# Kernel optimization log

Measured on AMD Instinct MI355X. Metric: run time of the kernel, lower is better.

## Reference

```python
import jax, jax.numpy as jnp
import numpy as np
from jax import lax

B = 1
D, H, W = 16, 16, 32
L = D * H * W
C = 96          # hidden_dim
DIN = 96        # d_inner = expansion_factor(1) * hidden_dim
N = 16          # d_state
R = 6           # dt_rank = ceil(C / 16)
K = 8           # scan directions: 4 axis orders x {fwd, bwd}
PERMS = [(0, 1, 2), (1, 2, 0), (2, 0, 1), (2, 1, 0)]


def _ln(x, w, b, eps):
    m = x.mean(-1, keepdims=True)
    v = ((x - m) ** 2).mean(-1, keepdims=True)
    return (x - m) * lax.rsqrt(v + eps) * w + b


def _conv3d(x, w, b, groups=1):
    y = lax.conv_general_dilated(x, w, (1, 1, 1), 'SAME', feature_group_count=groups,
                                 dimension_numbers=('NCDHW', 'OIDHW', 'NCDHW'))
    return y + b[None, :, None, None, None]


def _ss3d(x5, in_proj_w, conv_w, conv_b, x_proj_w, dt_w, dt_b, A_logs, Ds,
          out_norm_w, out_norm_b, out_proj_w):
    b, d, h, w, _ = x5.shape
    l = d * h * w
    spatial = (d, h, w)
    xz = jnp.einsum('bdhwc,ec->bdhwe', x5, in_proj_w)          # (b,d,h,w,2*DIN)
    x, z = jnp.split(xz, 2, axis=-1)
    x = jnp.transpose(x, (0, 4, 1, 2, 3))                       # (b,DIN,d,h,w)
    x = jax.nn.silu(_conv3d(x, conv_w, conv_b, groups=DIN))     # depthwise conv
    # build K/2 axis-order scans, then add reversed copies -> K directions
    xs = jnp.stack([jnp.transpose(x, (0, 1, 2 + p[0], 2 + p[1], 2 + p[2])).reshape(b, DIN, l)
                    for p in PERMS], axis=1)                    # (b,4,DIN,l)
    xs = jnp.concatenate([xs, jnp.flip(xs, -1)], axis=1)        # (b,K,DIN,l)
    x_dbl = jnp.einsum('bkdl,ked->bkel', xs, x_proj_w)          # e = R+2N
    dts, Bs, Cs = x_dbl[:, :, :R], x_dbl[:, :, R:R + N], x_dbl[:, :, R + N:]
    dts = jax.nn.softplus(jnp.einsum('bkrl,kdr->bkdl', dts, dt_w) + dt_b[None, :, :, None])
    A = -jnp.exp(A_logs)                                        # (K,DIN,N)
    # time-major for the selective scan
    dts_t = jnp.moveaxis(dts, -1, 0)                            # (l,b,K,DIN)
    xs_t = jnp.moveaxis(xs, -1, 0)
    Bs_t = jnp.moveaxis(Bs, -1, 0)                              # (l,b,K,N)
    Cs_t = jnp.moveaxis(Cs, -1, 0)

    def step(hc, inps):
        dt, u, Bt, Ct = inps
        hc = jnp.exp(dt[..., None] * A) * hc + (dt * u)[..., None] * Bt[:, :, None, :]
        y = jnp.einsum('bkdn,bkn->bkd', hc, Ct)
        return hc, y

    h0 = jnp.zeros((b, K, DIN, N), x.dtype)
    _, ys = lax.scan(step, h0, (dts_t, xs_t, Bs_t, Cs_t))       # ys: (l,b,K,DIN)
    ys = jnp.moveaxis(ys, 0, -1) + Ds[None, :, :, None] * xs    # (b,K,DIN,l)
    y_f, y_b = ys[:, :4], jnp.flip(ys[:, 4:], -1)
    acc = jnp.zeros((b, DIN, l), x.dtype)
    for i, p in enumerate(PERMS):
        inv = np.argsort(p)
        pshape = tuple(spatial[ax] for ax in p)
        for yk in (y_f[:, i], y_b[:, i]):
            yk = yk.reshape(b, DIN, *pshape)
            yk = jnp.transpose(yk, (0, 1, 2 + int(inv[0]), 2 + int(inv[1]), 2 + int(inv[2])))
            acc = acc + yk.reshape(b, DIN, l)
    y = _ln(jnp.transpose(acc, (0, 2, 1)), out_norm_w, out_norm_b, 1e-5)
    y = y.reshape(b, d, h, w, DIN) * jax.nn.silu(z)
    return jnp.einsum('bdhwe,ce->bdhwc', y, out_proj_w)


def _cab(x, cab_w1, cab_b1, cab_w2, cab_b2, ca_w1, ca_b1, ca_w2, ca_b2):
    # x: (b,C,d,h,w); conv -> GELU -> conv -> channel attention
    t = jax.nn.gelu(_conv3d(x, cab_w1, cab_b1), approximate=False)
    t = _conv3d(t, cab_w2, cab_b2)
    m = t.mean(axis=(2, 3, 4))                                  # global avg pool (b,C)
    v = jax.nn.relu(m @ ca_w1.T + ca_b1)
    v = jax.nn.sigmoid(v @ ca_w2.T + ca_b2)
    return t * v[:, :, None, None, None]


def _forward(inp, ln1_w, ln1_b, skip1, skip2, ln2_w, ln2_b, in_proj_w, conv_w, conv_b,
             x_proj_w, dt_w, dt_b, A_logs, Ds, out_norm_w, out_norm_b, out_proj_w,
             cab_w1, cab_b1, cab_w2, cab_b2, ca_w1, ca_b1, ca_w2, ca_b2, x_size):
    b, l, c = inp.shape
    d, h, w = x_size
    x5 = inp.reshape(b, d, h, w, c)
    xn = _ln(x5, ln1_w, ln1_b, 1e-6)
    attn = _ss3d(xn, in_proj_w, conv_w, conv_b, x_proj_w, dt_w, dt_b, A_logs, Ds,
                 out_norm_w, out_norm_b, out_proj_w)
    x = x5 * skip1 + attn                                       # drop_path = identity (rate 0)
    y2 = jnp.transpose(_ln(x, ln2_w, ln2_b, 1e-5), (0, 4, 1, 2, 3))
    cab = _cab(y2, cab_w1, cab_b1, cab_w2, cab_b2, ca_w1, ca_b1, ca_w2, ca_b2)
    x = x * skip2 + jnp.transpose(cab, (0, 2, 3, 4, 1))
    return x.reshape(b, l, c)


def setup_inputs() -> dict:
    key = jax.random.key(0)
    ks = jax.random.split(key, 12)
    g = lambda i, shp, s=0.02: jax.random.normal(ks[i], shp, jnp.float32) * s
    return {
        'inp': jax.random.normal(ks[0], (B, L, C), jnp.float32),
        'x_size': (D, H, W),
        'ln1_w': jnp.ones((C,), jnp.float32), 'ln1_b': jnp.zeros((C,), jnp.float32),
        'skip1': jnp.ones((C,), jnp.float32), 'skip2': jnp.ones((C,), jnp.float32),
        'ln2_w': jnp.ones((C,), jnp.float32), 'ln2_b': jnp.zeros((C,), jnp.float32),
        'in_proj_w': g(1, (2 * DIN, C)),
        'conv_w': g(2, (DIN, 1, 3, 3, 3), 0.1), 'conv_b': jnp.zeros((DIN,), jnp.float32),
        'x_proj_w': g(3, (K, R + 2 * N, DIN)),
        'dt_w': g(4, (K, DIN, R), 0.1), 'dt_b': g(5, (K, DIN), 0.1),
        'A_logs': jnp.log(jnp.tile(jnp.arange(1, N + 1, dtype=jnp.float32), (K, DIN, 1))),
        'Ds': jnp.ones((K, DIN), jnp.float32),
        'out_norm_w': jnp.ones((DIN,), jnp.float32), 'out_norm_b': jnp.zeros((DIN,), jnp.float32),
        'out_proj_w': g(6, (C, DIN)),
        'cab_w1': g(7, (C // 3, C, 3, 3, 3), 0.05), 'cab_b1': jnp.zeros((C // 3,), jnp.float32),
        'cab_w2': g(8, (C, C // 3, 3, 3, 3), 0.05), 'cab_b2': jnp.zeros((C,), jnp.float32),
        'ca_w1': g(9, (C // 2, C)), 'ca_b1': jnp.zeros((C // 2,), jnp.float32),
        'ca_w2': g(10, (C, C // 2)), 'ca_b2': jnp.zeros((C,), jnp.float32),
    }


def reference(inp, ln1_w, ln1_b, skip1, skip2, ln2_w, ln2_b, in_proj_w, conv_w, conv_b,
              x_proj_w, dt_w, dt_b, A_logs, Ds, out_norm_w, out_norm_b, out_proj_w,
              cab_w1, cab_b1, cab_w2, cab_b2, ca_w1, ca_b1, ca_w2, ca_b2, x_size):
    return _forward(inp, ln1_w, ln1_b, skip1, skip2, ln2_w, ln2_b, in_proj_w, conv_w, conv_b,
                    x_proj_w, dt_w, dt_b, A_logs, Ds, out_norm_w, out_norm_b, out_proj_w,
                    cab_w1, cab_b1, cab_w2, cab_b2, ca_w1, ca_b1, ca_w2, ca_b2, x_size)
```

## Files before the change

### kernel.cpp

```cpp
#include <hip/hip_runtime.h>
#include <math.h>

#define LL 8192
#define CC 96
#define DINc 96
#define NN 16
#define RR 6
#define KK 8
#define Dd 16
#define Hh 16
#define Ww 32
#define NCH 32
#define CHL 256

__constant__ int Pc_[4][3] = {{0,1,2},{1,2,0},{2,0,1},{2,1,0}};

__device__ __forceinline__ float silu_(float x){ return x / (1.f + __expf(-x)); }

__global__ void k_ln1(const float* __restrict__ inp, const float* __restrict__ w,
                      const float* __restrict__ b, float* __restrict__ xn_cm) {
    int l = blockIdx.x * blockDim.x + threadIdx.x;
    if (l >= LL) return;
    const float* p = inp + l * CC;
    float m = 0.f;
    for (int c = 0; c < CC; ++c) m += p[c];
    m *= (1.f / CC);
    float v = 0.f;
    for (int c = 0; c < CC; ++c) { float d = p[c] - m; v += d * d; }
    v *= (1.f / CC);
    float r = rsqrtf(v + 1e-6f);
    for (int c = 0; c < CC; ++c) xn_cm[c * LL + l] = (p[c] - m) * r * w[c] + b[c];
}

__global__ void k_wtrans(const float* __restrict__ inpj, const float* __restrict__ xpw,
                         const float* __restrict__ w1, const float* __restrict__ w2,
                         const float* __restrict__ opw,
                         float* __restrict__ ipT, float* __restrict__ xpT,
                         float* __restrict__ wT1, float* __restrict__ wT2,
                         float* __restrict__ opT) {
    int idx = blockIdx.x * blockDim.x + threadIdx.x;
    if (idx < 82944) {
        int oc = idx & 31; int tap = (idx >> 5) % 27; int ic = idx / (32 * 27);
        wT1[idx] = w1[(oc * 96 + ic) * 27 + tap];
    }
    if (idx < 82944) {
        int oc = idx % 96; int tap = (idx / 96) % 27; int ic = idx / (96 * 27);
        wT2[idx] = w2[(oc * 32 + ic) * 27 + tap];
    }
    if (idx < 18432) {
        int e = idx % 192; int c = idx / 192;
        ipT[idx] = inpj[e * 96 + c];
    }
    if (idx < 29184) {
        int e = idx % 38; int c = (idx / 38) % 96; int k = idx / (38 * 96);
        xpT[idx] = xpw[(k * 38 + e) * 96 + c];
    }
    if (idx < 9216) {
        int c = idx % 96; int e = idx / 96;
        opT[idx] = opw[c * 96 + e];
    }
}

__global__ void k_inproj(const float* __restrict__ xn_cm, const float* __restrict__ ipT,
                         float* __restrict__ xcm, float* __restrict__ z_rm) {
    int bx = blockIdx.x;
    int eb = bx >> 5;
    int l  = ((bx & 31) << 8) + threadIdx.x;
    int e0 = eb << 3;
    float a[8];
    #pragma unroll
    for (int j = 0; j < 8; ++j) a[j] = 0.f;
    const float* wp = ipT + e0;
    for (int c = 0; c < CC; ++c) {
        float x = xn_cm[c * LL + l];
        const float4* wv = (const float4*)(wp + c * 192);
        float4 wa = wv[0], wb = wv[1];
        a[0] += x * wa.x; a[1] += x * wa.y; a[2] += x * wa.z; a[3] += x * wa.w;
        a[4] += x * wb.x; a[5] += x * wb.y; a[6] += x * wb.z; a[7] += x * wb.w;
    }
    if (e0 < DINc) {
        float* dst = xcm + (long)e0 * LL;
        #pragma unroll
        for (int j = 0; j < 8; ++j) dst[(long)j * LL + l] = a[j];
    } else {
        float* dst = z_rm + (long)l * DINc + (e0 - DINc);
        #pragma unroll
        for (int j = 0; j < 8; ++j) dst[j] = a[j];
    }
}

__global__ void k_dwconv(const float* __restrict__ xcm, const float* __restrict__ cw,
                         const float* __restrict__ cb, float* __restrict__ xs0) {
    int bx = blockIdx.x;
    int c  = bx >> 3;
    int l4 = ((bx & 7) << 8) + threadIdx.x;
    int w0 = (l4 & 7) << 2;
    int h  = (l4 >> 3) & 15;
    int d  = l4 >> 7;
    int l  = (d * Hh + h) * Ww + w0;
    float wk[27];
    #pragma unroll
    for (int t = 0; t < 27; ++t) wk[t] = cw[c * 27 + t];
    float rmask[9]; int roff[9];
    #pragma unroll
    for (int kd = 0; kd < 3; ++kd) {
        int dd = d + kd - 1;
        bool vd = (unsigned)dd < Dd; int dc = vd ? dd : 0;
        #pragma unroll
        for (int kh = 0; kh < 3; ++kh) {
            int hh = h + kh - 1;
            bool vh = (unsigned)hh < Hh; int hcl = vh ? hh : 0;
            rmask[kd * 3 + kh] = (vd && vh) ? 1.f : 0.f;
            roff[kd * 3 + kh]  = (dc * Hh + hcl) * Ww + w0;
        }
    }
    float mleft  = (w0 > 0)  ? 1.f : 0.f;
    float mright = (w0 < 28) ? 1.f : 0.f;
    float a0 = cb[c], a1 = a0, a2 = a0, a3 = a0;
    const float* xp = xcm + (long)c * LL;
    #pragma unroll
    for (int r = 0; r < 9; ++r) {
        float rm = rmask[r];
        const float* xr = xp + roff[r];
        float4 xc = *(const float4*)xr;
        float v[6];
        v[0] = xr[-1] * (rm * mleft);
        v[1] = xc.x * rm; v[2] = xc.y * rm; v[3] = xc.z * rm; v[4] = xc.w * rm;
        v[5] = xr[4] * (rm * mright);
        #pragma unroll
        for (int t = 0; t < 3; ++t) {
            float wv = wk[r * 3 + t];
            a0 += v[t + 0] * wv;
            a1 += v[t + 1] * wv;
            a2 += v[t + 2] * wv;
            a3 += v[t + 3] * wv;
        }
    }
    *(float4*)(xs0 + (long)c * LL + l) = make_float4(silu_(a0), silu_(a1), silu_(a2), silu_(a3));
}

__global__ void k_permA(float* __restrict__ xs) {
    int idx = blockIdx.x * blockDim.x + threadIdx.x;
    if (idx >= 3 * DINc * LL) return;
    int l = idx & (LL - 1);
    int c = (idx >> 13) % DINc;
    int k = idx / (DINc * LL) + 1;
    int p0 = Pc_[k][0], p1 = Pc_[k][1], p2 = Pc_[k][2];
    const int sp[3] = {Dd, Hh, Ww};
    int pd1 = sp[p1], pd2 = sp[p2];
    int i2 = l % pd2;
    int t  = l / pd2;
    int i1 = t % pd1;
    int i0 = t / pd1;
    int coord[3];
    coord[p0] = i0; coord[p1] = i1; coord[p2] = i2;
    int o = (coord[0] * Hh + coord[1]) * Ww + coord[2];
    xs[(k * DINc + c) * LL + l] = xs[c * LL + o];
}

__global__ void k_permB(float* __restrict__ xs) {
    int idx = blockIdx.x * blockDim.x + threadIdx.x;
    if (idx >= 4 * DINc * (LL / 4)) return;
    int q = idx & (LL / 4 - 1);
    int c = (idx >> 11) % DINc;
    int k = idx / (DINc * (LL / 4));
    const float4* src = (const float4*)(xs + ((long)k * DINc + c) * LL);
    float4 s = src[LL / 4 - 1 - q];
    float4* dst = (float4*)(xs + ((long)(k + 4) * DINc + c) * LL);
    dst[q] = make_float4(s.w, s.z, s.y, s.x);
}

__global__ void k_xdbl(const float* __restrict__ xs, const float* __restrict__ xpT,
                       float* __restrict__ dtr, float* __restrict__ Bb, float* __restrict__ Cb) {
    int bx = blockIdx.x;
    int k = bx >> 5;
    int l = ((bx & 31) << 8) + threadIdx.x;
    float acc[38];
    #pragma unroll
    for (int e = 0; e < 38; ++e) acc[e] = 0.f;
    const float* xb = xs + (long)k * DINc * LL + l;
    const float* wb = xpT + k * DINc * 38;
    for (int c = 0; c < DINc; ++c) {
        float x = xb[(long)c * LL];
        const float* wr = wb + c * 38;
        #pragma unroll
        for (int e = 0; e < 38; ++e) acc[e] += x * wr[e];
    }
    float* dtp = dtr + ((long)k * LL + l) * 6;
    #pragma unroll
    for (int r = 0; r < RR; ++r) dtp[r] = acc[r];
    int lq = l >> 2, q = l & 3;
    float* Bp = Bb + (((long)k * 2048 + lq) * 16) * 4 + q;
    float* Cp = Cb + (((long)k * 2048 + lq) * 16) * 4 + q;
    #pragma unroll
    for (int n = 0; n < NN; ++n) { Bp[n * 4] = acc[RR + n]; Cp[n * 4] = acc[RR + NN + n]; }
}

__device__ __forceinline__ float softplus_(float x) {
    return (x > 20.f) ? x : __logf(1.f + __expf(x));
}

__global__ __launch_bounds__(512)
void k_scanf(float* __restrict__ xs_ys, const float* __restrict__ dtr,
             const float* __restrict__ Bb, const float* __restrict__ Cb,
             const float* __restrict__ A_logs, const float* __restrict__ dt_w,
             const float* __restrict__ dt_b, const float* __restrict__ Ds) {
    __shared__ __align__(16) float sdt[LL + (LL >> 7) * 4];
    __shared__ float sAp[16][33];
    __shared__ float sBc[16][33];
    __shared__ float shs[16][33];
    int bx = blockIdx.x;
    int grp = (bx & 7) * DINc + (bx >> 3);
    int k = grp / DINc;
    int tid = threadIdx.x;
    int n = tid & 15;
    int chunk = tid >> 4;
    {
        float w0 = dt_w[grp * RR + 0], w1 = dt_w[grp * RR + 1], w2 = dt_w[grp * RR + 2];
        float w3 = dt_w[grp * RR + 3], w4 = dt_w[grp * RR + 4], w5 = dt_w[grp * RR + 5];
        float dtb = dt_b[grp];
        const float* drb = dtr + (long)k * LL * 6;
        for (int i = tid; i < LL; i += 512) {
            const float2* dp = (const float2*)(drb + (long)i * 6);
            float2 d0 = dp[0], d1 = dp[1], d2 = dp[2];
            float dtl = dtb + d0.x * w0 + d0.y * w1 + d1.x * w2 + d1.y * w3 + d2.x * w4 + d2.y * w5;
            sdt[i + ((i >> 7) << 2)] = softplus_(dtl);
        }
    }
    __syncthreads();
    float A_n = -__expf(A_logs[grp * NN + n]);
    const float4* sdt4 = (const float4*)sdt;
    int dbase = chunk * 66;
    const float4* u4 = (const float4*)(xs_ys + (long)grp * LL + chunk * CHL);
    const float4* B4 = (const float4*)Bb + ((long)k * 2048 + chunk * (CHL / 4)) * 16 + n;
    const float4* C4 = (const float4*)Cb + ((long)k * 2048 + chunk * (CHL / 4)) * 16 + n;
    {
        float hc = 0.f, dsum = 0.f;
        #pragma unroll 4
        for (int q = 0; q < CHL / 4; ++q) {
            float4 dt = sdt4[dbase + q + (q >> 5)];
            float4 uu = u4[q];
            float4 Bv = B4[q * 16];
            dsum += (dt.x + dt.y) + (dt.z + dt.w);
            hc = __expf(dt.x * A_n) * hc + (dt.x * uu.x) * Bv.x;
            hc = __expf(dt.y * A_n) * hc + (dt.y * uu.y) * Bv.y;
            hc = __expf(dt.z * A_n) * hc + (dt.z * uu.z) * Bv.z;
            hc = __expf(dt.w * A_n) * hc + (dt.w * uu.w) * Bv.w;
        }
        sAp[n][chunk] = __expf(A_n * dsum);
        sBc[n][chunk] = hc;
    }
    __syncthreads();
    if (tid < 16) {
        float h = 0.f;
        for (int c = 0; c < NCH; ++c) {
            shs[tid][c] = h;
            h = sAp[tid][c] * h + sBc[tid][c];
        }
    }
    __syncthreads();
    float Dv = Ds[grp];
    float* urow = xs_ys + (long)grp * LL + chunk * CHL;
    float hc = shs[n][chunk];
    int qsel = n >> 2, csel = n & 3;
    bool b0 = (n & 1), b1 = ((n >> 1) & 1), b2 = ((n >> 2) & 1), b3 = (n >> 3);
    for (int base = 0; base < CHL; base += 16) {
        float u_lane = 0.f;
        float p[16];
        #pragma unroll
        for (int q = 0; q < 4; ++q) {
            int qq = (base >> 2) + q;
            float4 dt = sdt4[dbase + qq + (qq >> 5)];
            float4 uu = *(const float4*)(urow + base + q * 4);
            float4 Bv = B4[qq * 16];
            float4 Cv = C4[qq * 16];
            if (q == qsel)
                u_lane = (csel == 0) ? uu.x : (csel == 1) ? uu.y : (csel == 2) ? uu.z : uu.w;
            hc = __expf(dt.x * A_n) * hc + (dt.x * uu.x) * Bv.x;  p[q*4+0] = hc * Cv.x;
            hc = __expf(dt.y * A_n) * hc + (dt.y * uu.y) * Bv.y;  p[q*4+1] = hc * Cv.y;
            hc = __expf(dt.z * A_n) * hc + (dt.z * uu.z) * Bv.z;  p[q*4+2] = hc * Cv.z;
            hc = __expf(dt.w * A_n) * hc + (dt.w * uu.w) * Bv.w;  p[q*4+3] = hc * Cv.w;
        }
        float q8[8];
        #pragma unroll
        for (int m = 0; m < 8; ++m) {
            float sel = b0 ? p[2*m] : p[2*m+1];
            float r = __shfl_xor(sel, 1, 16);
            q8[m] = (b0 ? p[2*m+1] : p[2*m]) + r;
        }
        float r4[4];
        #pragma unroll
        for (int m = 0; m < 4; ++m) {
            float sel = b1 ? q8[2*m] : q8[2*m+1];
            float r = __shfl_xor(sel, 2, 16);
            r4[m] = (b1 ? q8[2*m+1] : q8[2*m]) + r;
        }
        float t2r[2];
        #pragma unroll
        for (int m = 0; m < 2; ++m) {
            float sel = b2 ? r4[2*m] : r4[2*m+1];
            float r = __shfl_xor(sel, 4, 16);
            t2r[m] = (b2 ? r4[2*m+1] : r4[2*m]) + r;
        }
        float sel = b3 ? t2r[0] : t2r[1];
        float r = __shfl_xor(sel, 8, 16);
        float yv = (b3 ? t2r[1] : t2r[0]) + r;
        urow[base + n] = yv + Dv * u_lane;
    }
}

__global__ void k_combproj(const float* __restrict__ ys, const float* __restrict__ z_rm,
                           const float* __restrict__ w, const float* __restrict__ b,
                           const float* __restrict__ opT, const float* __restrict__ inp,
                           const float* __restrict__ skip1, float* __restrict__ xafter) {
    __shared__ float sy[4][96];
    int wave = threadIdx.x >> 6;
    int lane = threadIdx.x & 63;
    int l = blockIdx.x * 4 + wave;
    int d = l >> 9, h = (l >> 5) & 15, wd = l & 31;
    int lps[4];
    lps[0] = l;
    lps[1] = (h * 32 + wd) * 16 + d;
    lps[2] = (wd * 16 + d) * 16 + h;
    lps[3] = (wd * 16 + h) * 16 + d;
    int c0 = lane, c1 = 64 + lane;
    float a0 = 0.f, a1 = 0.f;
    #pragma unroll
    for (int i = 0; i < 4; ++i) {
        a0 += ys[((long)(i * 96) + c0) * LL + lps[i]];
        a0 += ys[((long)((4 + i) * 96) + c0) * LL + (LL - 1 - lps[i])];
    }
    if (lane < 32) {
        #pragma unroll
        for (int i = 0; i < 4; ++i) {
            a1 += ys[((long)(i * 96) + c1) * LL + lps[i]];
            a1 += ys[((long)((4 + i) * 96) + c1) * LL + (LL - 1 - lps[i])];
        }
    }
    float s = a0 + a1;
    #pragma unroll
    for (int o = 1; o < 64; o <<= 1) s += __shfl_xor(s, o, 64);
    float m = s * (1.f / 96.f);
    float d0 = a0 - m;
    float d1 = (lane < 32) ? (a1 - m) : 0.f;
    float ss = d0 * d0 + d1 * d1;
    #pragma unroll
    for (int o = 1; o < 64; o <<= 1) ss += __shfl_xor(ss, o, 64);
    float r = rsqrtf(ss * (1.f / 96.f) + 1e-5f);
    float zz = z_rm[(long)l * 96 + c0];
    sy[wave][c0] = (d0 * r * w[c0] + b[c0]) * silu_(zz);
    if (lane < 32) {
        float z1 = z_rm[(long)l * 96 + c1];
        sy[wave][c1] = (d1 * r * w[c1] + b[c1]) * silu_(z1);
    }
    __syncthreads();
    int c1g = (lane < 32) ? c1 : 0;
    float o0 = 0.f, o1 = 0.f;
    #pragma unroll 4
    for (int e = 0; e < 96; ++e) {
        float ye = sy[wave][e];
        o0 += ye * opT[e * 96 + c0];
        o1 += ye * opT[e * 96 + c1g];
    }
    xafter[(long)l * 96 + c0] = inp[(long)l * 96 + c0] * skip1[c0] + o0;
    if (lane < 32)
        xafter[(long)l * 96 + c1] = inp[(long)l * 96 + c1] * skip1[c1] + o1;
}

__global__ void k_ln2(const float* __restrict__ xafter, const float* __restrict__ w,
                      const float* __restrict__ b, float* __restrict__ y2) {
    __shared__ float tile[16][97];
    __shared__ float smean[16], srstd[16];
    int l0 = blockIdx.x * 16;
    int tid = threadIdx.x;
    #pragma unroll
    for (int r = 0; r < 6; ++r) {
        int e = r * 256 + tid;
        int lo = e / 96, c = e % 96;
        tile[lo][c] = xafter[(long)(l0 + lo) * 96 + c];
    }
    __syncthreads();
    {
        int lo = tid >> 4, g = tid & 15;
        float ps = 0.f;
        #pragma unroll
        for (int j = 0; j < 6; ++j) ps += tile[lo][g * 6 + j];
        #pragma unroll
        for (int o = 1; o < 16; o <<= 1) ps += __shfl_xor(ps, o, 16);
        float m = ps * (1.f / 96.f);
        float pv = 0.f;
        #pragma unroll
        for (int j = 0; j < 6; ++j) { float dd = tile[lo][g * 6 + j] - m; pv += dd * dd; }
        #pragma unroll
        for (int o = 1; o < 16; o <<= 1) pv += __shfl_xor(pv, o, 16);
        if (g == 0) { smean[lo] = m; srstd[lo] = rsqrtf(pv * (1.f / 96.f) + 1e-5f); }
    }
    __syncthreads();
    #pragma unroll
    for (int r = 0; r < 6; ++r) {
        int e = r * 256 + tid;
        int c = e >> 4, lo = e & 15;
        y2[(long)c * LL + l0 + lo] = (tile[lo][c] - smean[lo]) * srstd[lo] * w[c] + b[c];
    }
}

__global__ void k_conv1(const float* __restrict__ y2, const float* __restrict__ wT,
                        float* __restrict__ part) {
    int bx = blockIdx.x;
    int g  = bx >> 3;
    int ocg = g & 3;
    int isp = g >> 2;
    int l4 = ((bx & 7) << 8) + threadIdx.x;
    int w0 = (l4 & 7) << 2;
    int h  = (l4 >> 3) & 15;
    int d  = l4 >> 7;
    int l  = (d * Hh + h) * Ww + w0;
    float rmask[9]; int roff[9];
    #pragma unroll
    for (int kd = 0; kd < 3; ++kd) {
        int dd = d + kd - 1;
        bool vd = (unsigned)dd < Dd; int dc = vd ? dd : 0;
        #pragma unroll
        for (int kh = 0; kh < 3; ++kh) {
            int hh = h + kh - 1;
            bool vh = (unsigned)hh < Hh; int hcl = vh ? hh : 0;
            rmask[kd * 3 + kh] = (vd && vh) ? 1.f : 0.f;
            roff[kd * 3 + kh]  = (dc * Hh + hcl) * Ww + w0;
        }
    }
    float mleft  = (w0 > 0)  ? 1.f : 0.f;
    float mright = (w0 < 28) ? 1.f : 0.f;
    float acc[32];
    #pragma unroll
    for (int j = 0; j < 32; ++j) acc[j] = 0.f;
    for (int ic = isp * 6; ic < isp * 6 + 6; ++ic) {
        const float* xp = y2 + (long)ic * LL;
        const float* wb = wT + ic * 864 + ocg * 8;
        #pragma unroll
        for (int r = 0; r < 9; ++r) {
            float rm = rmask[r];
            const float* xr = xp + roff[r];
            float4 xc = *(const float4*)xr;
            float v[6];
            v[0] = xr[-1] * (rm * mleft);
            v[1] = xc.x * rm; v[2] = xc.y * rm; v[3] = xc.z * rm; v[4] = xc.w * rm;
            v[5] = xr[4] * (rm * mright);
            #pragma unroll
            for (int t = 0; t < 3; ++t) {
                const float4* wv = (const float4*)(wb + (r * 3 + t) * 32);
                float4 wa = wv[0], wbv = wv[1];
                #pragma unroll
                for (int p = 0; p < 4; ++p) {
                    float x = v[t + p];
                    acc[0  + p] += x * wa.x;  acc[4  + p] += x * wa.y;
                    acc[8  + p] += x * wa.z;  acc[12 + p] += x * wa.w;
                    acc[16 + p] += x * wbv.x; acc[20 + p] += x * wbv.y;
                    acc[24 + p] += x * wbv.z; acc[28 + p] += x * wbv.w;
                }
            }
        }
    }
    float* pp = part + ((long)(isp * 32 + ocg * 8)) * LL + l;
    #pragma unroll
    for (int oc = 0; oc < 8; ++oc)
        *(float4*)(pp + (long)oc * LL) = make_float4(acc[oc*4+0], acc[oc*4+1], acc[oc*4+2], acc[oc*4+3]);
}

__global__ void k_gelusum(const float* __restrict__ part, const float* __restrict__ b1,
                          float* __restrict__ t1) {
    int idx = blockIdx.x * blockDim.x + threadIdx.x;
    if (idx >= 32 * LL) return;
    int l = idx & (LL - 1);
    int oc = idx >> 13;
    float s = b1[oc];
    #pragma unroll
    for (int isp = 0; isp < 16; ++isp)
        s += part[((long)(isp * 32 + oc)) * LL + l];
    t1[oc * LL + l] = 0.5f * s * (1.f + erff(s * 0.70710678118654752f));
}

__global__ void k_conv2(const float* __restrict__ t1, const float* __restrict__ wT,
                        float* __restrict__ part) {
    int bx = blockIdx.x;
    int g  = bx >> 3;
    int ocg = g % 12;
    int isp = g / 12;
    int l4 = ((bx & 7) << 8) + threadIdx.x;
    int w0 = (l4 & 7) << 2;
    int h  = (l4 >> 3) & 15;
    int d  = l4 >> 7;
    int l  = (d * Hh + h) * Ww + w0;
    float rmask[9]; int roff[9];
    #pragma unroll
    for (int kd = 0; kd < 3; ++kd) {
        int dd = d + kd - 1;
        bool vd = (unsigned)dd < Dd; int dc = vd ? dd : 0;
        #pragma unroll
        for (int kh = 0; kh < 3; ++kh) {
            int hh = h + kh - 1;
            bool vh = (unsigned)hh < Hh; int hcl = vh ? hh : 0;
            rmask[kd * 3 + kh] = (vd && vh) ? 1.f : 0.f;
            roff[kd * 3 + kh]  = (dc * Hh + hcl) * Ww + w0;
        }
    }
    float mleft  = (w0 > 0)  ? 1.f : 0.f;
    float mright = (w0 < 28) ? 1.f : 0.f;
    float acc[32];
    #pragma unroll
    for (int j = 0; j < 32; ++j) acc[j] = 0.f;
    for (int ic = isp * 4; ic < isp * 4 + 4; ++ic) {
        const float* xp = t1 + (long)ic * LL;
        const float* wb = wT + ic * 2592 + ocg * 8;
        #pragma unroll
        for (int r = 0; r < 9; ++r) {
            float rm = rmask[r];
            const float* xr = xp + roff[r];
            float4 xc = *(const float4*)xr;
            float v[6];
            v[0] = xr[-1] * (rm * mleft);
            v[1] = xc.x * rm; v[2] = xc.y * rm; v[3] = xc.z * rm; v[4] = xc.w * rm;
            v[5] = xr[4] * (rm * mright);
            #pragma unroll
            for (int t = 0; t < 3; ++t) {
                const float4* wv = (const float4*)(wb + (r * 3 + t) * 96);
                float4 wa = wv[0], wbv = wv[1];
                #pragma unroll
                for (int p = 0; p < 4; ++p) {
                    float x = v[t + p];
                    acc[0  + p] += x * wa.x;  acc[4  + p] += x * wa.y;
                    acc[8  + p] += x * wa.z;  acc[12 + p] += x * wa.w;
                    acc[16 + p] += x * wbv.x; acc[20 + p] += x * wbv.y;
                    acc[24 + p] += x * wbv.z; acc[28 + p] += x * wbv.w;
                }
            }
        }
    }
    float* pp = part + ((long)(isp * 96 + ocg * 8)) * LL + l;
    #pragma unroll
    for (int oc = 0; oc < 8; ++oc)
        *(float4*)(pp + (long)oc * LL) = make_float4(acc[oc*4+0], acc[oc*4+1], acc[oc*4+2], acc[oc*4+3]);
}

__global__ void k_conv2sum(const float* __restrict__ part, const float* __restrict__ b2,
                           float* __restrict__ t2) {
    int idx = blockIdx.x * blockDim.x + threadIdx.x;
    if (idx >= 96 * LL) return;
    int l = idx & (LL - 1);
    int oc = idx >> 13;
    float s = b2[oc];
    #pragma unroll
    for (int isp = 0; isp < 8; ++isp)
        s += part[((long)(isp * 96 + oc)) * LL + l];
    t2[oc * LL + l] = s;
}

__global__ void k_mean(const float* __restrict__ t2, float* __restrict__ mbuf) {
    __shared__ float sm[256];
    int c = blockIdx.x;
    const float4* tp = (const float4*)(t2 + (long)c * LL);
    float a = 0.f;
    for (int q = threadIdx.x; q < LL / 4; q += 256) {
        float4 v = tp[q];
        a += (v.x + v.y) + (v.z + v.w);
    }
    sm[threadIdx.x] = a;
    __syncthreads();
    for (int o = 128; o > 0; o >>= 1) {
        if (threadIdx.x < o) sm[threadIdx.x] += sm[threadIdx.x + o];
        __syncthreads();
    }
    if (threadIdx.x == 0) mbuf[c] = sm[0] * (1.f / LL);
}

__global__ void k_mlp(const float* __restrict__ mbuf, const float* __restrict__ w1,
                      const float* __restrict__ b1, const float* __restrict__ w2,
                      const float* __restrict__ b2, float* __restrict__ v2) {
    __shared__ float v[48];
    int t = threadIdx.x;
    if (t < 48) {
        float s = b1[t];
        for (int c = 0; c < 96; ++c) s += mbuf[c] * w1[t * 96 + c];
        v[t] = fmaxf(s, 0.f);
    }
    __syncthreads();
    if (t < 96) {
        float s = b2[t];
        for (int j = 0; j < 48; ++j) s += v[j] * w2[t * 48 + j];
        v2[t] = 1.f / (1.f + __expf(-s));
    }
}

__global__ void k_final(const float* __restrict__ xafter, const float* __restrict__ skip2,
                        const float* __restrict__ t2, const float* __restrict__ v2,
                        float* __restrict__ out) {
    __shared__ float tile[96][17];
    __shared__ float sk2[96], sv2[96];
    int l0 = blockIdx.x * 16;
    int tid = threadIdx.x;
    if (tid < 96) { sk2[tid] = skip2[tid]; sv2[tid] = v2[tid]; }
    #pragma unroll
    for (int r = 0; r < 6; ++r) {
        int e = r * 256 + tid;
        int c = e >> 4, lo = e & 15;
        tile[c][lo] = t2[(long)c * LL + l0 + lo];
    }
    __syncthreads();
    #pragma unroll
    for (int r = 0; r < 6; ++r) {
        int e = r * 256 + tid;
        int lo = e / 96, c = e % 96;
        long gi = (long)(l0 + lo) * 96 + c;
        out[gi] = xafter[gi] * sk2[c] + tile[c][lo] * sv2[c];
    }
}

static const size_t OFF_XS     = 0;
static const size_t OFF_Z      = 6291456;
static const size_t OFF_XCM    = 7077888;
static const size_t OFF_XN     = 7864320;
static const size_t OFF_DTRAW  = 8650752;
static const size_t OFF_BB     = 9043968;
static const size_t OFF_CB     = 10092544;
static const size_t OFF_XAFTER = 11141120;
static const size_t OFF_Y2     = 11927552;
static const size_t OFF_T1     = 12713984;
static const size_t OFF_T2     = 12976128;
static const size_t OFF_MV     = 13762560;
static const size_t OFF_WT1    = 13762816;
static const size_t OFF_WT2    = 13845760;
static const size_t OFF_IPT    = 13928704;
static const size_t OFF_XPT    = 13947136;
static const size_t OFF_OPT    = 13976320;

extern "C" void kernel_launch(void* const* d_in, const int* in_sizes, int n_in,
                              void* d_out, int out_size, void* d_ws, size_t ws_size,
                              hipStream_t stream) {
    const float* inp    = (const float*)d_in[0];
    const float* ln1_w  = (const float*)d_in[2];
    const float* ln1_b  = (const float*)d_in[3];
    const float* skip1  = (const float*)d_in[4];
    const float* skip2  = (const float*)d_in[5];
    const float* ln2_w  = (const float*)d_in[6];
    const float* ln2_b  = (const float*)d_in[7];
    const float* inpj   = (const float*)d_in[8];
    const float* conv_w = (const float*)d_in[9];
    const float* conv_b = (const float*)d_in[10];
    const float* xpw    = (const float*)d_in[11];
    const float* dt_w   = (const float*)d_in[12];
    const float* dt_b   = (const float*)d_in[13];
    const float* A_logs = (const float*)d_in[14];
    const float* Ds     = (const float*)d_in[15];
    const float* onw    = (const float*)d_in[16];
    const float* onb    = (const float*)d_in[17];
    const float* opw    = (const float*)d_in[18];
    const float* cab_w1 = (const float*)d_in[19];
    const float* cab_b1 = (const float*)d_in[20];
    const float* cab_w2 = (const float*)d_in[21];
    const float* cab_b2 = (const float*)d_in[22];
    const float* ca_w1  = (const float*)d_in[23];
    const float* ca_b1  = (const float*)d_in[24];
    const float* ca_w2  = (const float*)d_in[25];
    const float* ca_b2  = (const float*)d_in[26];

    float* ws = (float*)d_ws;
    float* xs     = ws + OFF_XS;
    float* zbuf   = ws + OFF_Z;
    float* xcm    = ws + OFF_XCM;
    float* xn     = ws + OFF_XN;
    float* dtr    = ws + OFF_DTRAW;
    float* Bb     = ws + OFF_BB;
    float* Cb     = ws + OFF_CB;
    float* xafter = ws + OFF_XAFTER;
    float* y2     = ws + OFF_Y2;
    float* t1     = ws + OFF_T1;
    float* t2     = ws + OFF_T2;
    float* mv     = ws + OFF_MV;
    float* wT1    = ws + OFF_WT1;
    float* wT2    = ws + OFF_WT2;
    float* ipT    = ws + OFF_IPT;
    float* xpT    = ws + OFF_XPT;
    float* opT    = ws + OFF_OPT;
    float* part1  = xs;
    float* part2  = xs;

    float* out = (float*)d_out;
    #define GRID(n) dim3((unsigned)(((n) + 255) / 256)), dim3(256)

    hipLaunchKernelGGL(k_ln1,     GRID(LL),                   0, stream, inp, ln1_w, ln1_b, xn);
    hipLaunchKernelGGL(k_wtrans,  GRID(82944),                0, stream, inpj, xpw, cab_w1, cab_w2, opw, ipT, xpT, wT1, wT2, opT);
    hipLaunchKernelGGL(k_inproj,  dim3(768), dim3(256),       0, stream, xn, ipT, xcm, zbuf);
    hipLaunchKernelGGL(k_dwconv,  dim3(768), dim3(256),       0, stream, xcm, conv_w, conv_b, xs);
    hipLaunchKernelGGL(k_permA,   GRID(3 * DINc * LL),        0, stream, xs);
    hipLaunchKernelGGL(k_permB,   GRID(4 * DINc * (LL / 4)),  0, stream, xs);
    hipLaunchKernelGGL(k_xdbl,    dim3(256), dim3(256),       0, stream, xs, xpT, dtr, Bb, Cb);
    hipLaunchKernelGGL(k_scanf,   dim3(KK * DINc), dim3(512), 0, stream, xs, dtr, Bb, Cb, A_logs, dt_w, dt_b, Ds);
    hipLaunchKernelGGL(k_combproj,dim3(LL / 4), dim3(256),    0, stream, xs, zbuf, onw, onb, opT, inp, skip1, xafter);
    hipLaunchKernelGGL(k_ln2,     dim3(512), dim3(256),       0, stream, xafter, ln2_w, ln2_b, y2);
    hipLaunchKernelGGL(k_conv1,   dim3(512), dim3(256),       0, stream, y2, wT1, part1);
    hipLaunchKernelGGL(k_gelusum, GRID(32 * LL),              0, stream, part1, cab_b1, t1);
    hipLaunchKernelGGL(k_conv2,   dim3(768), dim3(256),       0, stream, t1, wT2, part2);
    hipLaunchKernelGGL(k_conv2sum,GRID(96 * LL),              0, stream, part2, cab_b2, t2);
    hipLaunchKernelGGL(k_mean,    dim3(96), dim3(256),        0, stream, t2, mv);
    hipLaunchKernelGGL(k_mlp,     dim3(1), dim3(128),         0, stream, mv, ca_w1, ca_b1, ca_w2, ca_b2, mv + 96);
    hipLaunchKernelGGL(k_final,   dim3(512), dim3(256),       0, stream, xafter, skip2, t2, mv + 96, out);
    #undef GRID
}
```

Baseline: 306.7 us.

## Tile LN1 and axis permutation through shared memory, split x_proj outputs

LayerNorm1 now stages 16 tokens in shared memory and uses shuffle reductions, so both the reads and the channel-major writes are coalesced. The axis permutation stages each full channel (8192 floats, padded against bank conflicts) in LDS and gathers from there instead of scattering global reads. x_dbl splits its 38 outputs into two halves over twice as many blocks to raise occupancy. The cost is redundant x loads in x_dbl and the large LDS footprint in permA.

Result: faster. 298.0 us (-2.8%).

```diff
diff --git a/kernel.cpp b/kernel.cpp
--- a/kernel.cpp
+++ b/kernel.cpp
@@ -19,17 +19,39 @@
 
 __global__ void k_ln1(const float* __restrict__ inp, const float* __restrict__ w,
                       const float* __restrict__ b, float* __restrict__ xn_cm) {
-    int l = blockIdx.x * blockDim.x + threadIdx.x;
-    if (l >= LL) return;
-    const float* p = inp + l * CC;
-    float m = 0.f;
-    for (int c = 0; c < CC; ++c) m += p[c];
-    m *= (1.f / CC);
-    float v = 0.f;
-    for (int c = 0; c < CC; ++c) { float d = p[c] - m; v += d * d; }
-    v *= (1.f / CC);
-    float r = rsqrtf(v + 1e-6f);
-    for (int c = 0; c < CC; ++c) xn_cm[c * LL + l] = (p[c] - m) * r * w[c] + b[c];
+    __shared__ float tile[16][97];
+    __shared__ float smean[16], srstd[16];
+    int l0 = blockIdx.x * 16;
+    int tid = threadIdx.x;
+    #pragma unroll
+    for (int r = 0; r < 6; ++r) {
+        int e = r * 256 + tid;
+        int lo = e / 96, c = e % 96;
+        tile[lo][c] = inp[(long)(l0 + lo) * 96 + c];
+    }
+    __syncthreads();
+    {
+        int lo = tid >> 4, g = tid & 15;
+        float ps = 0.f;
+        #pragma unroll
+        for (int j = 0; j < 6; ++j) ps += tile[lo][g * 6 + j];
+        #pragma unroll
+        for (int o = 1; o < 16; o <<= 1) ps += __shfl_xor(ps, o, 16);
+        float m = ps * (1.f / 96.f);
+        float pv = 0.f;
+        #pragma unroll
+        for (int j = 0; j < 6; ++j) { float dd = tile[lo][g * 6 + j] - m; pv += dd * dd; }
+        #pragma unroll
+        for (int o = 1; o < 16; o <<= 1) pv += __shfl_xor(pv, o, 16);
+        if (g == 0) { smean[lo] = m; srstd[lo] = rsqrtf(pv * (1.f / 96.f) + 1e-6f); }
+    }
+    __syncthreads();
+    #pragma unroll
+    for (int r = 0; r < 6; ++r) {
+        int e = r * 256 + tid;
+        int c = e >> 4, lo = e & 15;
+        xn_cm[(long)c * LL + l0 + lo] = (tile[lo][c] - smean[lo]) * srstd[lo] * w[c] + b[c];
+    }
 }
 
 __global__ void k_wtrans(const float* __restrict__ inpj, const float* __restrict__ xpw,
@@ -140,22 +162,29 @@
 }
 
 __global__ void k_permA(float* __restrict__ xs) {
-    int idx = blockIdx.x * blockDim.x + threadIdx.x;
-    if (idx >= 3 * DINc * LL) return;
-    int l = idx & (LL - 1);
-    int c = (idx >> 13) % DINc;
-    int k = idx / (DINc * LL) + 1;
+    __shared__ float lv[8192 + 256 + 16];
+    int bx = blockIdx.x;
+    int k = bx / 96 + 1;
+    int c = bx % 96;
+    const float* src = xs + (long)c * LL;
+    float* dst = xs + ((long)k * DINc + c) * LL;
+    int tid = threadIdx.x;
+    for (int i = tid; i < LL; i += 256)
+        lv[i + (i >> 5) + (i >> 9)] = src[i];
+    __syncthreads();
     int p0 = Pc_[k][0], p1 = Pc_[k][1], p2 = Pc_[k][2];
     const int sp[3] = {Dd, Hh, Ww};
     int pd1 = sp[p1], pd2 = sp[p2];
-    int i2 = l % pd2;
-    int t  = l / pd2;
-    int i1 = t % pd1;
-    int i0 = t / pd1;
-    int coord[3];
-    coord[p0] = i0; coord[p1] = i1; coord[p2] = i2;
-    int o = (coord[0] * Hh + coord[1]) * Ww + coord[2];
-    xs[(k * DINc + c) * LL + l] = xs[c * LL + o];
+    for (int i = tid; i < LL; i += 256) {
+        int i2 = i % pd2;
+        int t  = i / pd2;
+        int i1 = t % pd1;
+        int i0 = t / pd1;
+        int coord[3];
+        coord[p0] = i0; coord[p1] = i1; coord[p2] = i2;
+        int o = (coord[0] * Hh + coord[1]) * Ww + coord[2];
+        dst[i] = lv[o + (o >> 5) + (o >> 9)];
+    }
 }
 
 __global__ void k_permB(float* __restrict__ xs) {
@@ -173,27 +202,34 @@
 __global__ void k_xdbl(const float* __restrict__ xs, const float* __restrict__ xpT,
                        float* __restrict__ dtr, float* __restrict__ Bb, float* __restrict__ Cb) {
     int bx = blockIdx.x;
-    int k = bx >> 5;
-    int l = ((bx & 31) << 8) + threadIdx.x;
-    float acc[38];
-    #pragma unroll
-    for (int e = 0; e < 38; ++e) acc[e] = 0.f;
+    int k = bx >> 6;
+    int rest = bx & 63;
+    int eh = rest & 1;
+    int lblk = rest >> 1;
+    int l = (lblk << 8) + threadIdx.x;
+    int e0 = eh * 19;
+    float acc[19];
+    #pragma unroll
+    for (int e = 0; e < 19; ++e) acc[e] = 0.f;
     const float* xb = xs + (long)k * DINc * LL + l;
-    const float* wb = xpT + k * DINc * 38;
+    const float* wb = xpT + k * DINc * 38 + e0;
     for (int c = 0; c < DINc; ++c) {
         float x = xb[(long)c * LL];
         const float* wr = wb + c * 38;
         #pragma unroll
-        for (int e = 0; e < 38; ++e) acc[e] += x * wr[e];
-    }
-    float* dtp = dtr + ((long)k * LL + l) * 6;
-    #pragma unroll
-    for (int r = 0; r < RR; ++r) dtp[r] = acc[r];
+        for (int e = 0; e < 19; ++e) acc[e] += x * wr[e];
+    }
     int lq = l >> 2, q = l & 3;
-    float* Bp = Bb + (((long)k * 2048 + lq) * 16) * 4 + q;
-    float* Cp = Cb + (((long)k * 2048 + lq) * 16) * 4 + q;
-    #pragma unroll
-    for (int n = 0; n < NN; ++n) { Bp[n * 4] = acc[RR + n]; Cp[n * 4] = acc[RR + NN + n]; }
+    #pragma unroll
+    for (int e = 0; e < 19; ++e) {
+        int ge = e0 + e;
+        if (ge < RR)
+            dtr[((long)k * LL + l) * 6 + ge] = acc[e];
+        else if (ge < RR + NN)
+            Bb[(((long)k * 2048 + lq) * 16 + (ge - RR)) * 4 + q] = acc[e];
+        else
+            Cb[(((long)k * 2048 + lq) * 16 + (ge - RR - NN)) * 4 + q] = acc[e];
+    }
 }
 
 __device__ __forceinline__ float softplus_(float x) {
@@ -686,13 +722,13 @@
     float* out = (float*)d_out;
     #define GRID(n) dim3((unsigned)(((n) + 255) / 256)), dim3(256)
 
-    hipLaunchKernelGGL(k_ln1,     GRID(LL),                   0, stream, inp, ln1_w, ln1_b, xn);
+    hipLaunchKernelGGL(k_ln1,     dim3(512), dim3(256),       0, stream, inp, ln1_w, ln1_b, xn);
     hipLaunchKernelGGL(k_wtrans,  GRID(82944),                0, stream, inpj, xpw, cab_w1, cab_w2, opw, ipT, xpT, wT1, wT2, opT);
     hipLaunchKernelGGL(k_inproj,  dim3(768), dim3(256),       0, stream, xn, ipT, xcm, zbuf);
     hipLaunchKernelGGL(k_dwconv,  dim3(768), dim3(256),       0, stream, xcm, conv_w, conv_b, xs);
-    hipLaunchKernelGGL(k_permA,   GRID(3 * DINc * LL),        0, stream, xs);
+    hipLaunchKernelGGL(k_permA,   dim3(288), dim3(256),       0, stream, xs);
     hipLaunchKernelGGL(k_permB,   GRID(4 * DINc * (LL / 4)),  0, stream, xs);
-    hipLaunchKernelGGL(k_xdbl,    dim3(256), dim3(256),       0, stream, xs, xpT, dtr, Bb, Cb);
+    hipLaunchKernelGGL(k_xdbl,    dim3(512), dim3(256),       0, stream, xs, xpT, dtr, Bb, Cb);
     hipLaunchKernelGGL(k_scanf,   dim3(KK * DINc), dim3(512), 0, stream, xs, dtr, Bb, Cb, A_logs, dt_w, dt_b, Ds);
     hipLaunchKernelGGL(k_combproj,dim3(LL / 4), dim3(256),    0, stream, xs, zbuf, onw, onb, opT, inp, skip1, xafter);
     hipLaunchKernelGGL(k_ln2,     dim3(512), dim3(256),       0, stream, xafter, ln2_w, ln2_b, y2);
```
